# Optimization experiments

Measured on AMD Instinct MI355X. Metric: run time of the kernel, lower is better.

## Reference

```python
import jax, jax.numpy as jnp
import numpy as np

B, C, Q, H = 16, 1024, 128, 768  # batch, context_len, query_len, hidden (= proj_size)


def setup_inputs() -> dict:
    key = jax.random.key(0)
    ks = jax.random.split(key, 8)
    s = 1.0 / np.sqrt(H)
    return {
        "context": jax.random.normal(ks[0], (B, C, H), jnp.float32),
        "context_masks": jnp.ones((B, C), jnp.float32),
        "query": jax.random.normal(ks[1], (B, Q, H), jnp.float32),
        "query_masks": jnp.ones((B, Q), jnp.float32),
        "Wc": jax.random.uniform(ks[2], (H, H), jnp.float32, -s, s),   # proj_ctx weight [out,in]
        "bc": jax.random.uniform(ks[3], (H,), jnp.float32, -s, s),
        "Wq": jax.random.uniform(ks[4], (H, H), jnp.float32, -s, s),   # proj_ques weight
        "bq": jax.random.uniform(ks[5], (H,), jnp.float32, -s, s),
        "w_att": jax.random.uniform(ks[6], (H,), jnp.float32, -s, s),  # attention Linear(H,1) weight
        "b_att": jax.random.uniform(ks[7], (), jnp.float32, -s, s),
    }


def reference(context, context_masks, query, query_masks, Wc, bc, Wq, bq, w_att, b_att):
    # Projections (dropout rate = 0 -> identity)
    ctx = jnp.einsum("bch,ph->bcp", context, Wc) + bc          # [B,C,H]
    qry = jnp.einsum("bqh,ph->bqp", query, Wq) + bq            # [B,Q,H]

    # sim[b,c,q] = sum_p w_att[p]*ctx[b,c,p]*qry[b,q,p] + b_att
    # (algebraic collapse of repeat + elementwise-mul + Linear(H,1))
    sim = jnp.einsum("bcp,bqp->bcq", ctx * w_att, qry) + b_att  # [B,C,Q]

    alpha = jax.nn.softmax(sim, axis=-1)
    alpha = alpha * context_masks[:, :, None] * query_masks[:, None, :]
    a = jnp.einsum("bcq,bqp->bcp", alpha, qry)                  # [B,C,H]

    q2c = jnp.max(sim, axis=-1)                                 # [B,C]
    beta = jax.nn.softmax(q2c, axis=-1) * context_masks         # [B,C]
    b = jnp.einsum("bc,bcp->bp", beta, ctx)                     # [B,H]

    c = ctx * a
    d = ctx * b[:, None, :]
    return jnp.concatenate([ctx, a, c, d], axis=-1)             # [B,C,4H]
```

## Files before the change

### kernel.cpp

```cpp
#include <hip/hip_runtime.h>
#include <cstdint>

#define B_ 16
#define C_ 1024
#define Q_ 128
#define H_ 768
#define OSTR (4 * H_)

typedef __attribute__((ext_vector_type(8))) short bf16x8;
typedef __attribute__((ext_vector_type(4))) float f32x4;
typedef __attribute__((ext_vector_type(4))) int int4v;

__device__ __forceinline__ unsigned short f2bf(float x) {
  union { float f; unsigned u; } v; v.f = x;
  unsigned r = v.u + 0x7FFFu + ((v.u >> 16) & 1u);
  return (unsigned short)(r >> 16);
}
__device__ __forceinline__ unsigned pk2(float a, float b) {
  return (unsigned)f2bf(a) | ((unsigned)f2bf(b) << 16);
}
__device__ __forceinline__ float bf2f(unsigned short u) {
  union { unsigned u; float f; } t; t.u = ((unsigned)u) << 16; return t.f;
}

__global__ __launch_bounds__(256) void f2bf4_kernel(
    const float* __restrict__ s0, unsigned short* __restrict__ d0, int n0,
    const float* __restrict__ s1, unsigned short* __restrict__ d1, int n1,
    const float* __restrict__ s2, unsigned short* __restrict__ d2, int n2,
    const float* __restrict__ s3, unsigned short* __restrict__ d3, int n3) {
  int i = blockIdx.x * 256 + threadIdx.x;
  const float* s;
  unsigned short* d;
  if (i < n0) { s = s0; d = d0; }
  else if ((i -= n0) < n1) { s = s1; d = d1; }
  else if ((i -= n1) < n2) { s = s2; d = d2; }
  else if ((i -= n2) < n3) { s = s3; d = d3; }
  else return;
  f32x4 a = __builtin_nontemporal_load((const f32x4*)s + 2 * i);
  f32x4 b = __builtin_nontemporal_load((const f32x4*)s + 2 * i + 1);
  int4v o;
  o[0] = (int)pk2(a[0], a[1]); o[1] = (int)pk2(a[2], a[3]);
  o[2] = (int)pk2(b[0], b[1]); o[3] = (int)pk2(b[2], b[3]);
  ((int4v*)d)[i] = o;
}

template <int MODE>
__global__ __launch_bounds__(256) void gemm_uni(
    const unsigned short* __restrict__ A, const unsigned short* __restrict__ Bm,
    const float* __restrict__ bias, unsigned short* __restrict__ ob1,
    unsigned short* __restrict__ ob2, const float* __restrict__ watt,
    const float* __restrict__ cmask, const float* __restrict__ qmask,
    float* __restrict__ q2c, int K, int qchunk) {
  __shared__ __align__(16) unsigned char smem[(MODE == 0) ? 33792 : 16384];
  __shared__ float pmS[2][64];
  __shared__ float psS[2][64];
  constexpr int AROWS = (MODE < 2) ? 128 : 64;
  constexpr int MI = (MODE < 2) ? 4 : 2;
  unsigned short* As = (unsigned short*)smem;
  unsigned short* Ws = (unsigned short*)(smem + ((MODE < 2) ? 8192 : 4096));
  const int tid = threadIdx.x;
  const int lane = tid & 63;
  const int w = tid >> 6;
  const int orig = ((int)blockIdx.x & 7) * qchunk + ((int)blockIdx.x >> 3);
  const int wrA = (w >> 1) * (AROWS / 2);
  const int wcB = (w & 1) * 64;
  const int fr = lane & 15;
  const int fq = lane >> 4;

  int gm, gn, bb;
  const unsigned short *Ap, *Bp;
  if constexpr (MODE == 0 || MODE == 1) {
    gm = (orig / 6) * 128; gn = (orig % 6) * 128; bb = 0;
    Ap = A + (size_t)gm * K; Bp = Bm + (size_t)gn * K;
  } else {
    bb = orig >> 4; gm = bb * C_ + (orig & 15) * 64; gn = 0;
    Ap = A + (size_t)gm * K; Bp = Bm + (size_t)bb * Q_ * K;
  }

  auto stage128 = [&](const unsigned short* __restrict__ G, unsigned short* S, int k0) {
#pragma unroll
    for (int r = 0; r < 2; ++r) {
      const int c = r * 256 + tid;
      const int row = c >> 2, sub = c & 3;
      const unsigned short* g = G + (size_t)row * K + k0 + sub * 8;
      unsigned short* l = S + (size_t)(r * 256 + w * 64) * 8;
      __builtin_amdgcn_global_load_lds(
          (const __attribute__((address_space(1))) void*)g,
          (__attribute__((address_space(3))) void*)l, 16, 0, 0);
    }
  };
  auto stage64 = [&](const unsigned short* __restrict__ G, unsigned short* S, int k0) {
    const int c = tid;
    const int row = c >> 2, sub = c & 3;
    const unsigned short* g = G + (size_t)row * K + k0 + sub * 8;
    unsigned short* l = S + (size_t)(w * 64) * 8;
    __builtin_amdgcn_global_load_lds(
        (const __attribute__((address_space(1))) void*)g,
        (__attribute__((address_space(3))) void*)l, 16, 0, 0);
  };

  f32x4 acc[MI][4];
#pragma unroll
  for (int i = 0; i < MI; ++i)
#pragma unroll
    for (int j = 0; j < 4; ++j)
#pragma unroll
      for (int e = 0; e < 4; ++e) acc[i][j][e] = 0.f;

  for (int k0 = 0; k0 < K; k0 += 32) {
    if constexpr (MODE < 2) stage128(Ap, As, k0); else stage64(Ap, As, k0);
    stage128(Bp, Ws, k0);
    __syncthreads();
    bf16x8 af[MI], wf[4];
#pragma unroll
    for (int i = 0; i < MI; ++i)
      af[i] = *(const bf16x8*)(As + (wrA + i * 16 + fr) * 32 + fq * 8);
#pragma unroll
    for (int j = 0; j < 4; ++j)
      wf[j] = *(const bf16x8*)(Ws + (wcB + j * 16 + fr) * 32 + fq * 8);
#pragma unroll
    for (int i = 0; i < MI; ++i)
#pragma unroll
      for (int j = 0; j < 4; ++j)
        acc[i][j] = __builtin_amdgcn_mfma_f32_16x16x32_bf16(af[i], wf[j], acc[i][j], 0, 0, 0);
    __syncthreads();
  }

  if constexpr (MODE == 0) {
    unsigned short* tr16 = (unsigned short*)smem;
    float bj[4];
#pragma unroll
    for (int j = 0; j < 4; ++j) bj[j] = bias[gn + wcB + j * 16 + fr];
#pragma unroll
    for (int i = 0; i < 4; ++i)
#pragma unroll
      for (int j = 0; j < 4; ++j)
#pragma unroll
        for (int r = 0; r < 4; ++r)
          tr16[(wrA + i * 16 + fq * 4 + r) * 132 + wcB + j * 16 + fr] =
              f2bf(acc[i][j][r] + bj[j]);
    __syncthreads();
#pragma unroll
    for (int k = 0; k < 8; ++k) {
      const int f = k * 256 + tid;
      const int row = f >> 4, c8 = (f & 15) << 3;
      int4v v = *(const int4v*)&tr16[row * 132 + c8];
      *(int4v*)&ob1[(size_t)(gm + row) * H_ + gn + c8] = v;
    }
  } else if constexpr (MODE == 1) {
#pragma unroll
    for (int i = 0; i < 4; ++i) {
#pragma unroll
      for (int j = 0; j < 4; ++j) {
        const int n = gn + wcB + j * 16 + fr;
        const float bias_n = bias[n];
        const float wv = watt[n];
        ushort4 t4;
#pragma unroll
        for (int r = 0; r < 4; ++r) {
          const size_t m = (size_t)gm + wrA + i * 16 + fq * 4 + r;
          float v = acc[i][j][r] + bias_n;
          ob1[m * H_ + n] = f2bf(v * wv);
          (&t4.x)[r] = f2bf(v);
        }
        const int bidx = gm >> 7;
        const int q0 = wrA + i * 16 + fq * 4;
        *(ushort4*)(ob2 + ((size_t)bidx * H_ + n) * Q_ + q0) = t4;
      }
    }
  } else {
    float red[MI][4];
#pragma unroll
    for (int i = 0; i < MI; ++i)
#pragma unroll
      for (int r = 0; r < 4; ++r) {
        float mx = acc[i][0][r];
#pragma unroll
        for (int j = 1; j < 4; ++j) mx = fmaxf(mx, acc[i][j][r]);
        mx = fmaxf(mx, __shfl_xor(mx, 1));
        mx = fmaxf(mx, __shfl_xor(mx, 2));
        mx = fmaxf(mx, __shfl_xor(mx, 4));
        mx = fmaxf(mx, __shfl_xor(mx, 8));
        if (fr == 0) pmS[w & 1][wrA + i * 16 + fq * 4 + r] = mx;
      }
    __syncthreads();
    float qm[4];
#pragma unroll
    for (int j = 0; j < 4; ++j) qm[j] = qmask[bb * Q_ + wcB + j * 16 + fr];
#pragma unroll
    for (int i = 0; i < MI; ++i)
#pragma unroll
      for (int r = 0; r < 4; ++r) {
        const int lr = wrA + i * 16 + fq * 4 + r;
        const float M = fmaxf(pmS[0][lr], pmS[1][lr]);
        if ((w & 1) == 0 && fr == 0) q2c[gm + lr] = M;
        float s = 0.f;
#pragma unroll
        for (int j = 0; j < 4; ++j) {
          acc[i][j][r] = __expf(acc[i][j][r] - M);
          s += acc[i][j][r];
        }
        s += __shfl_xor(s, 1); s += __shfl_xor(s, 2);
        s += __shfl_xor(s, 4); s += __shfl_xor(s, 8);
        if (fr == 0) psS[w & 1][lr] = s;
      }
    __syncthreads();
#pragma unroll
    for (int i = 0; i < MI; ++i)
#pragma unroll
      for (int r = 0; r < 4; ++r) {
        const int lr = wrA + i * 16 + fq * 4 + r;
        const float S = psS[0][lr] + psS[1][lr];
        const float inv = cmask[gm + lr] / S;
#pragma unroll
        for (int j = 0; j < 4; ++j) {
          const int lc = wcB + j * 16 + fr;
          ob1[(size_t)(gm + lr) * Q_ + lc] = f2bf(acc[i][j][r] * inv * qm[j]);
        }
      }
  }
}

__global__ __launch_bounds__(256) void pv_kernel(
    const unsigned short* __restrict__ alpha, const unsigned short* __restrict__ qryT,
    const unsigned short* __restrict__ ctxp, const float* __restrict__ bvec,
    float* __restrict__ out32) {
  __shared__ __align__(16) unsigned char smem[33792];
  const int tid = threadIdx.x;
  const int lane = tid & 63;
  const int w = tid >> 6;
  const int fr = lane & 15;
  const int fq = lane >> 4;
  const int orig = ((int)blockIdx.x & 7) * 192 + ((int)blockIdx.x >> 3);
  const int bb = orig / 96;
  const int rem = orig % 96;
  const int gm = bb * C_ + (rem / 6) * 64;
  const int gn = (rem % 6) * 128;
  const unsigned short* Ap = alpha + (size_t)gm * Q_;
  const unsigned short* Bp = qryT + ((size_t)bb * H_ + gn) * Q_;
  const int wrA = (w >> 1) * 32;
  const int wcB = (w & 1) * 64;
  unsigned short* Ws = (unsigned short*)smem;

#pragma unroll
  for (int kk = 0; kk < 4; ++kk) {
#pragma unroll
    for (int r = 0; r < 2; ++r) {
      const int c = r * 256 + tid;
      const int row = c >> 2, sub = c & 3;
      const unsigned short* g = Bp + (size_t)row * Q_ + kk * 32 + sub * 8;
      unsigned short* l = Ws + kk * 4096 + (size_t)(r * 256 + w * 64) * 8;
      __builtin_amdgcn_global_load_lds(
          (const __attribute__((address_space(1))) void*)g,
          (__attribute__((address_space(3))) void*)l, 16, 0, 0);
    }
  }
  ushort4 cxr[8];
#pragma unroll
  for (int k = 0; k < 8; ++k) {
    const int f = k * 256 + tid;
    const int row = f >> 5, c4 = (f & 31) << 2;
    cxr[k] = *(const ushort4*)&ctxp[(size_t)(gm + row) * H_ + gn + c4];
  }
  bf16x8 af[2][4];
#pragma unroll
  for (int i = 0; i < 2; ++i)
#pragma unroll
    for (int kk = 0; kk < 4; ++kk)
      af[i][kk] = *(const bf16x8*)(Ap + (size_t)(wrA + i * 16 + fr) * Q_ + kk * 32 + fq * 8);

  f32x4 acc[2][4];
#pragma unroll
  for (int i = 0; i < 2; ++i)
#pragma unroll
    for (int j = 0; j < 4; ++j)
#pragma unroll
      for (int e = 0; e < 4; ++e) acc[i][j][e] = 0.f;

  __syncthreads();
#pragma unroll
  for (int kk = 0; kk < 4; ++kk) {
    bf16x8 wf[4];
#pragma unroll
    for (int j = 0; j < 4; ++j)
      wf[j] = *(const bf16x8*)(Ws + kk * 4096 + (wcB + j * 16 + fr) * 32 + fq * 8);
#pragma unroll
    for (int i = 0; i < 2; ++i)
#pragma unroll
      for (int j = 0; j < 4; ++j)
        acc[i][j] = __builtin_amdgcn_mfma_f32_16x16x32_bf16(af[i][kk], wf[j], acc[i][j], 0, 0, 0);
  }
  __syncthreads();

  float* tr = (float*)smem;
#pragma unroll
  for (int i = 0; i < 2; ++i)
#pragma unroll
    for (int j = 0; j < 4; ++j)
#pragma unroll
      for (int r = 0; r < 4; ++r)
        tr[(wrA + i * 16 + fq * 4 + r) * 132 + wcB + j * 16 + fr] = acc[i][j][r];
  __syncthreads();
#pragma unroll
  for (int k = 0; k < 8; ++k) {
    const int f = k * 256 + tid;
    const int row = f >> 5, c4 = (f & 31) << 2;
    f32x4 av = *(const f32x4*)&tr[row * 132 + c4];
    const ushort4 cu = cxr[k];
    f32x4 bv = *(const f32x4*)&bvec[bb * H_ + gn + c4];
    const float cx0 = bf2f(cu.x), cx1 = bf2f(cu.y), cx2 = bf2f(cu.z), cx3 = bf2f(cu.w);
    float* rowp = out32 + (size_t)(gm + row) * OSTR + gn;
    f32x4 cxv; cxv[0] = cx0; cxv[1] = cx1; cxv[2] = cx2; cxv[3] = cx3;
    __builtin_nontemporal_store(cxv, (f32x4*)&rowp[c4]);
    __builtin_nontemporal_store(av, (f32x4*)&rowp[H_ + c4]);
    f32x4 cc;
    cc[0] = cx0 * av[0]; cc[1] = cx1 * av[1]; cc[2] = cx2 * av[2]; cc[3] = cx3 * av[3];
    __builtin_nontemporal_store(cc, (f32x4*)&rowp[2 * H_ + c4]);
    f32x4 dd;
    dd[0] = cx0 * bv[0]; dd[1] = cx1 * bv[1]; dd[2] = cx2 * bv[2]; dd[3] = cx3 * bv[3];
    __builtin_nontemporal_store(dd, (f32x4*)&rowp[3 * H_ + c4]);
  }
}

__global__ __launch_bounds__(256) void beta_bvec_kernel(
    const unsigned short* __restrict__ ctxp, const float* __restrict__ q2c,
    const float* __restrict__ cmask, float* __restrict__ bvec) {
  __shared__ float sh[C_];
  __shared__ float red[256];
  const int tid = threadIdx.x;
  const int b = blockIdx.x / 12;
  const int p0 = (blockIdx.x % 12) * 64;
  float v[4];
  float lm = -1e30f;
#pragma unroll
  for (int i = 0; i < 4; ++i) {
    v[i] = q2c[b * C_ + i * 256 + tid];
    lm = fmaxf(lm, v[i]);
  }
  red[tid] = lm;
  __syncthreads();
  for (int off = 128; off > 0; off >>= 1) {
    if (tid < off) red[tid] = fmaxf(red[tid], red[tid + off]);
    __syncthreads();
  }
  const float m = red[0];
  __syncthreads();
  float ls = 0.f;
#pragma unroll
  for (int i = 0; i < 4; ++i) {
    float e = __expf(v[i] - m);
    sh[i * 256 + tid] = e * cmask[b * C_ + i * 256 + tid];
    ls += e;
  }
  red[tid] = ls;
  __syncthreads();
  for (int off = 128; off > 0; off >>= 1) {
    if (tid < off) red[tid] += red[tid + off];
    __syncthreads();
  }
  const float denom = red[0];
  const int pp = tid & 63;
  const int cg = tid >> 6;
  const unsigned short* base = ctxp + ((size_t)(b * C_ + cg)) * H_ + p0 + pp;
  float acc = 0.f;
#pragma unroll 4
  for (int c = cg; c < C_; c += 4) {
    acc += sh[c] * bf2f(*base);
    base += (size_t)4 * H_;
  }
  __syncthreads();
  red[tid] = acc;
  __syncthreads();
  if (tid < 64)
    bvec[b * H_ + p0 + tid] =
        (red[tid] + red[tid + 64] + red[tid + 128] + red[tid + 192]) / denom;
}

extern "C" void kernel_launch(void* const* d_in, const int* in_sizes, int n_in,
                              void* d_out, int out_size, void* d_ws, size_t ws_size,
                              hipStream_t stream) {
  const float* context = (const float*)d_in[0];
  const float* cmask   = (const float*)d_in[1];
  const float* query   = (const float*)d_in[2];
  const float* qmask   = (const float*)d_in[3];
  const float* Wc      = (const float*)d_in[4];
  const float* bc      = (const float*)d_in[5];
  const float* Wq      = (const float*)d_in[6];
  const float* bq      = (const float*)d_in[7];
  const float* w_att   = (const float*)d_in[8];
  float* out = (float*)d_out;

  unsigned short* ws_ctxb = (unsigned short*)d_ws;
  unsigned short* ws_qinb = ws_ctxb + (size_t)B_ * C_ * H_;
  unsigned short* ws_Wcb  = ws_qinb + (size_t)B_ * Q_ * H_;
  unsigned short* ws_Wqb  = ws_Wcb + (size_t)H_ * H_;
  unsigned short* ws_qryW = ws_Wqb + (size_t)H_ * H_;
  unsigned short* ws_qryT = ws_qryW + (size_t)B_ * Q_ * H_;
  unsigned short* ws_ctxp = ws_qryT + (size_t)B_ * H_ * Q_;
  float* ws_q2c  = (float*)(ws_ctxp + (size_t)B_ * C_ * H_);
  float* ws_bvec = ws_q2c + (size_t)B_ * C_;
  unsigned short* ws_alpha = ws_qinb;

  {
    const int n0 = B_ * C_ * H_ / 8;
    const int n1 = B_ * Q_ * H_ / 8;
    const int n2 = H_ * H_ / 8;
    const int n3 = n2;
    const int tot = n0 + n1 + n2 + n3;
    f2bf4_kernel<<<(tot + 255) / 256, 256, 0, stream>>>(
        context, ws_ctxb, n0, query, ws_qinb, n1, Wc, ws_Wcb, n2, Wq, ws_Wqb, n3);
  }
  gemm_uni<1><<<96, 256, 0, stream>>>(
      ws_qinb, ws_Wqb, bq, ws_qryW, ws_qryT, w_att,
      nullptr, nullptr, nullptr, H_, 12);
  gemm_uni<0><<<768, 256, 0, stream>>>(
      ws_ctxb, ws_Wcb, bc, ws_ctxp, nullptr, nullptr,
      nullptr, nullptr, nullptr, H_, 96);
  gemm_uni<2><<<256, 256, 0, stream>>>(
      ws_ctxp, ws_qryW, nullptr, ws_alpha, nullptr, nullptr,
      cmask, qmask, ws_q2c, H_, 32);
  beta_bvec_kernel<<<B_ * 12, 256, 0, stream>>>(ws_ctxp, ws_q2c, cmask, ws_bvec);
  pv_kernel<<<1536, 256, 0, stream>>>(ws_alpha, ws_qryT, ws_ctxp, ws_bvec, out);
}
```

Measured before the change: 155.1 us.

## Merge context and query projections into one launch; halve pv_kernel tile rows

The two projection GEMMs (context and query) now run as a single 864-block kernel that picks its operands by block index, so one launch replaces two and the 96 query blocks fill gaps alongside the 768 context blocks. The similarity/softmax GEMM is split out into its own specialised kernel with no logic change. pv_kernel now uses 32-row tiles instead of 64, doubling the grid to 3072 blocks and using fewer registers per block, which should help occupancy. In exchange, each Wq/qryT tile is reloaded into shared memory twice as often, and the merged kernel has a runtime branch on block role.

```diff
diff --git a/kernel.cpp b/kernel.cpp
--- a/kernel.cpp
+++ b/kernel.cpp
@@ -44,89 +44,79 @@
   ((int4v*)d)[i] = o;
 }
 
-template <int MODE>
-__global__ __launch_bounds__(256) void gemm_uni(
-    const unsigned short* __restrict__ A, const unsigned short* __restrict__ Bm,
-    const float* __restrict__ bias, unsigned short* __restrict__ ob1,
-    unsigned short* __restrict__ ob2, const float* __restrict__ watt,
-    const float* __restrict__ cmask, const float* __restrict__ qmask,
-    float* __restrict__ q2c, int K, int qchunk) {
-  __shared__ __align__(16) unsigned char smem[(MODE == 0) ? 33792 : 16384];
-  __shared__ float pmS[2][64];
-  __shared__ float psS[2][64];
-  constexpr int AROWS = (MODE < 2) ? 128 : 64;
-  constexpr int MI = (MODE < 2) ? 4 : 2;
+__global__ __launch_bounds__(256) void proj_kernel(
+    const unsigned short* __restrict__ ctxb, const unsigned short* __restrict__ Wcb,
+    const float* __restrict__ bc, unsigned short* __restrict__ ctxp,
+    const unsigned short* __restrict__ qinb, const unsigned short* __restrict__ Wqb,
+    const float* __restrict__ bq, unsigned short* __restrict__ qryW,
+    unsigned short* __restrict__ qryT, const float* __restrict__ watt) {
+  __shared__ __align__(16) unsigned char smem[33792];
   unsigned short* As = (unsigned short*)smem;
-  unsigned short* Ws = (unsigned short*)(smem + ((MODE < 2) ? 8192 : 4096));
+  unsigned short* Ws = (unsigned short*)(smem + 8192);
   const int tid = threadIdx.x;
   const int lane = tid & 63;
   const int w = tid >> 6;
-  const int orig = ((int)blockIdx.x & 7) * qchunk + ((int)blockIdx.x >> 3);
-  const int wrA = (w >> 1) * (AROWS / 2);
+  const int bid = (int)blockIdx.x;
+  const bool isC = bid < 768;
+  int orig, gm, gn;
+  const unsigned short *Ap, *Bp;
+  const float* bias;
+  if (isC) {
+    orig = (bid & 7) * 96 + (bid >> 3);
+    gm = (orig / 6) * 128; gn = (orig % 6) * 128;
+    Ap = ctxb + (size_t)gm * H_; Bp = Wcb + (size_t)gn * H_; bias = bc;
+  } else {
+    const int b2 = bid - 768;
+    orig = (b2 & 7) * 12 + (b2 >> 3);
+    gm = (orig / 6) * 128; gn = (orig % 6) * 128;
+    Ap = qinb + (size_t)gm * H_; Bp = Wqb + (size_t)gn * H_; bias = bq;
+  }
+  const int wrA = (w >> 1) * 64;
   const int wcB = (w & 1) * 64;
   const int fr = lane & 15;
   const int fq = lane >> 4;
 
-  int gm, gn, bb;
-  const unsigned short *Ap, *Bp;
-  if constexpr (MODE == 0 || MODE == 1) {
-    gm = (orig / 6) * 128; gn = (orig % 6) * 128; bb = 0;
-    Ap = A + (size_t)gm * K; Bp = Bm + (size_t)gn * K;
-  } else {
-    bb = orig >> 4; gm = bb * C_ + (orig & 15) * 64; gn = 0;
-    Ap = A + (size_t)gm * K; Bp = Bm + (size_t)bb * Q_ * K;
-  }
-
   auto stage128 = [&](const unsigned short* __restrict__ G, unsigned short* S, int k0) {
 #pragma unroll
     for (int r = 0; r < 2; ++r) {
       const int c = r * 256 + tid;
       const int row = c >> 2, sub = c & 3;
-      const unsigned short* g = G + (size_t)row * K + k0 + sub * 8;
+      const unsigned short* g = G + (size_t)row * H_ + k0 + sub * 8;
       unsigned short* l = S + (size_t)(r * 256 + w * 64) * 8;
       __builtin_amdgcn_global_load_lds(
           (const __attribute__((address_space(1))) void*)g,
           (__attribute__((address_space(3))) void*)l, 16, 0, 0);
     }
   };
-  auto stage64 = [&](const unsigned short* __restrict__ G, unsigned short* S, int k0) {
-    const int c = tid;
-    const int row = c >> 2, sub = c & 3;
-    const unsigned short* g = G + (size_t)row * K + k0 + sub * 8;
-    unsigned short* l = S + (size_t)(w * 64) * 8;
-    __builtin_amdgcn_global_load_lds(
-        (const __attribute__((address_space(1))) void*)g,
-        (__attribute__((address_space(3))) void*)l, 16, 0, 0);
-  };
-
-  f32x4 acc[MI][4];
-#pragma unroll
-  for (int i = 0; i < MI; ++i)
+
+  f32x4 acc[4][4];
+#pragma unroll
+  for (int i = 0; i < 4; ++i)
 #pragma unroll
     for (int j = 0; j < 4; ++j)
 #pragma unroll
       for (int e = 0; e < 4; ++e) acc[i][j][e] = 0.f;
 
-  for (int k0 = 0; k0 < K; k0 += 32) {
-    if constexpr (MODE < 2) stage128(Ap, As, k0); else stage64(Ap, As, k0);
+  for (int k0 = 0; k0 < H_; k0 += 32) {
+    stage128(Ap, As, k0);
     stage128(Bp, Ws, k0);
     __syncthreads();
-    bf16x8 af[MI], wf[4];
-#pragma unroll
-    for (int i = 0; i < MI; ++i)
+    bf16x8 af[4], wf[4];
+#pragma unroll
+    for (int i = 0; i < 4; ++i)
       af[i] = *(const bf16x8*)(As + (wrA + i * 16 + fr) * 32 + fq * 8);
 #pragma unroll
     for (int j = 0; j < 4; ++j)
       wf[j] = *(const bf16x8*)(Ws + (wcB + j * 16 + fr) * 32 + fq * 8);
 #pragma unroll
-    for (int i = 0; i < MI; ++i)
+    for (int i = 0; i < 4; ++i)
 #pragma unroll
       for (int j = 0; j < 4; ++j)
         acc[i][j] = __builtin_amdgcn_mfma_f32_16x16x32_bf16(af[i], wf[j], acc[i][j], 0, 0, 0);
     __syncthreads();
   }
 
-  if constexpr (MODE == 0) {
+  if (isC) {
     unsigned short* tr16 = (unsigned short*)smem;
     float bj[4];
 #pragma unroll
@@ -145,9 +135,9 @@
       const int f = k * 256 + tid;
       const int row = f >> 4, c8 = (f & 15) << 3;
       int4v v = *(const int4v*)&tr16[row * 132 + c8];
-      *(int4v*)&ob1[(size_t)(gm + row) * H_ + gn + c8] = v;
-    }
-  } else if constexpr (MODE == 1) {
+      *(int4v*)&ctxp[(size_t)(gm + row) * H_ + gn + c8] = v;
+    }
+  } else {
 #pragma unroll
     for (int i = 0; i < 4; ++i) {
 #pragma unroll
@@ -160,65 +150,131 @@
         for (int r = 0; r < 4; ++r) {
           const size_t m = (size_t)gm + wrA + i * 16 + fq * 4 + r;
           float v = acc[i][j][r] + bias_n;
-          ob1[m * H_ + n] = f2bf(v * wv);
+          qryW[m * H_ + n] = f2bf(v * wv);
           (&t4.x)[r] = f2bf(v);
         }
         const int bidx = gm >> 7;
         const int q0 = wrA + i * 16 + fq * 4;
-        *(ushort4*)(ob2 + ((size_t)bidx * H_ + n) * Q_ + q0) = t4;
+        *(ushort4*)(qryT + ((size_t)bidx * H_ + n) * Q_ + q0) = t4;
       }
     }
-  } else {
-    float red[MI][4];
-#pragma unroll
-    for (int i = 0; i < MI; ++i)
-#pragma unroll
-      for (int r = 0; r < 4; ++r) {
-        float mx = acc[i][0][r];
-#pragma unroll
-        for (int j = 1; j < 4; ++j) mx = fmaxf(mx, acc[i][j][r]);
-        mx = fmaxf(mx, __shfl_xor(mx, 1));
-        mx = fmaxf(mx, __shfl_xor(mx, 2));
-        mx = fmaxf(mx, __shfl_xor(mx, 4));
-        mx = fmaxf(mx, __shfl_xor(mx, 8));
-        if (fr == 0) pmS[w & 1][wrA + i * 16 + fq * 4 + r] = mx;
+  }
+}
+
+__global__ __launch_bounds__(256) void sim_kernel(
+    const unsigned short* __restrict__ A, const unsigned short* __restrict__ Bm,
+    unsigned short* __restrict__ alpha, const float* __restrict__ cmask,
+    const float* __restrict__ qmask, float* __restrict__ q2c) {
+  __shared__ __align__(16) unsigned char smem[16384];
+  __shared__ float pmS[2][64];
+  __shared__ float psS[2][64];
+  unsigned short* As = (unsigned short*)smem;
+  unsigned short* Ws = (unsigned short*)(smem + 4096);
+  const int tid = threadIdx.x;
+  const int lane = tid & 63;
+  const int w = tid >> 6;
+  const int orig = ((int)blockIdx.x & 7) * 32 + ((int)blockIdx.x >> 3);
+  const int bb = orig >> 4;
+  const int gm = bb * C_ + (orig & 15) * 64;
+  const int wrA = (w >> 1) * 32;
+  const int wcB = (w & 1) * 64;
+  const int fr = lane & 15;
+  const int fq = lane >> 4;
+  const unsigned short* Ap = A + (size_t)gm * H_;
+  const unsigned short* Bp = Bm + (size_t)bb * Q_ * H_;
+
+  f32x4 acc[2][4];
+#pragma unroll
+  for (int i = 0; i < 2; ++i)
+#pragma unroll
+    for (int j = 0; j < 4; ++j)
+#pragma unroll
+      for (int e = 0; e < 4; ++e) acc[i][j][e] = 0.f;
+
+  for (int k0 = 0; k0 < H_; k0 += 32) {
+    {
+      const int row = tid >> 2, sub = tid & 3;
+      const unsigned short* g = Ap + (size_t)row * H_ + k0 + sub * 8;
+      unsigned short* l = As + (size_t)(w * 64) * 8;
+      __builtin_amdgcn_global_load_lds(
+          (const __attribute__((address_space(1))) void*)g,
+          (__attribute__((address_space(3))) void*)l, 16, 0, 0);
+    }
+#pragma unroll
+    for (int r = 0; r < 2; ++r) {
+      const int c = r * 256 + tid;
+      const int row = c >> 2, sub = c & 3;
+      const unsigned short* g = Bp + (size_t)row * H_ + k0 + sub * 8;
+      unsigned short* l = Ws + (size_t)(r * 256 + w * 64) * 8;
+      __builtin_amdgcn_global_load_lds(
+          (const __attribute__((address_space(1))) void*)g,
+          (__attribute__((address_space(3))) void*)l, 16, 0, 0);
+    }
+    __syncthreads();
+    bf16x8 af[2], wf[4];
+#pragma unroll
+    for (int i = 0; i < 2; ++i)
+      af[i] = *(const bf16x8*)(As + (wrA + i * 16 + fr) * 32 + fq * 8);
+#pragma unroll
+    for (int j = 0; j < 4; ++j)
+      wf[j] = *(const bf16x8*)(Ws + (wcB + j * 16 + fr) * 32 + fq * 8);
+#pragma unroll
+    for (int i = 0; i < 2; ++i)
+#pragma unroll
+      for (int j = 0; j < 4; ++j)
+        acc[i][j] = __builtin_amdgcn_mfma_f32_16x16x32_bf16(af[i], wf[j], acc[i][j], 0, 0, 0);
+    __syncthreads();
+  }
+
+  float red[2][4];
+#pragma unroll
+  for (int i = 0; i < 2; ++i)
+#pragma unroll
+    for (int r = 0; r < 4; ++r) {
+      float mx = acc[i][0][r];
+#pragma unroll
+      for (int j = 1; j < 4; ++j) mx = fmaxf(mx, acc[i][j][r]);
+      mx = fmaxf(mx, __shfl_xor(mx, 1));
+      mx = fmaxf(mx, __shfl_xor(mx, 2));
+      mx = fmaxf(mx, __shfl_xor(mx, 4));
+      mx = fmaxf(mx, __shfl_xor(mx, 8));
+      if (fr == 0) pmS[w & 1][wrA + i * 16 + fq * 4 + r] = mx;
+    }
+  __syncthreads();
+  float qm[4];
+#pragma unroll
+  for (int j = 0; j < 4; ++j) qm[j] = qmask[bb * Q_ + wcB + j * 16 + fr];
+#pragma unroll
+  for (int i = 0; i < 2; ++i)
+#pragma unroll
+    for (int r = 0; r < 4; ++r) {
+      const int lr = wrA + i * 16 + fq * 4 + r;
+      const float M = fmaxf(pmS[0][lr], pmS[1][lr]);
+      if ((w & 1) == 0 && fr == 0) q2c[gm + lr] = M;
+      float s = 0.f;
+#pragma unroll
+      for (int j = 0; j < 4; ++j) {
+        acc[i][j][r] = __expf(acc[i][j][r] - M);
+        s += acc[i][j][r];
       }
-    __syncthreads();
-    float qm[4];
-#pragma unroll
-    for (int j = 0; j < 4; ++j) qm[j] = qmask[bb * Q_ + wcB + j * 16 + fr];
-#pragma unroll
-    for (int i = 0; i < MI; ++i)
-#pragma unroll
-      for (int r = 0; r < 4; ++r) {
-        const int lr = wrA + i * 16 + fq * 4 + r;
-        const float M = fmaxf(pmS[0][lr], pmS[1][lr]);
-        if ((w & 1) == 0 && fr == 0) q2c[gm + lr] = M;
-        float s = 0.f;
-#pragma unroll
-        for (int j = 0; j < 4; ++j) {
-          acc[i][j][r] = __expf(acc[i][j][r] - M);
-          s += acc[i][j][r];
-        }
-        s += __shfl_xor(s, 1); s += __shfl_xor(s, 2);
-        s += __shfl_xor(s, 4); s += __shfl_xor(s, 8);
-        if (fr == 0) psS[w & 1][lr] = s;
+      s += __shfl_xor(s, 1); s += __shfl_xor(s, 2);
+      s += __shfl_xor(s, 4); s += __shfl_xor(s, 8);
+      if (fr == 0) psS[w & 1][lr] = s;
+    }
+  __syncthreads();
+#pragma unroll
+  for (int i = 0; i < 2; ++i)
+#pragma unroll
+    for (int r = 0; r < 4; ++r) {
+      const int lr = wrA + i * 16 + fq * 4 + r;
+      const float S = psS[0][lr] + psS[1][lr];
+      const float inv = cmask[gm + lr] / S;
+#pragma unroll
+      for (int j = 0; j < 4; ++j) {
+        const int lc = wcB + j * 16 + fr;
+        alpha[(size_t)(gm + lr) * Q_ + lc] = f2bf(acc[i][j][r] * inv * qm[j]);
       }
-    __syncthreads();
-#pragma unroll
-    for (int i = 0; i < MI; ++i)
-#pragma unroll
-      for (int r = 0; r < 4; ++r) {
-        const int lr = wrA + i * 16 + fq * 4 + r;
-        const float S = psS[0][lr] + psS[1][lr];
-        const float inv = cmask[gm + lr] / S;
-#pragma unroll
-        for (int j = 0; j < 4; ++j) {
-          const int lc = wcB + j * 16 + fr;
-          ob1[(size_t)(gm + lr) * Q_ + lc] = f2bf(acc[i][j][r] * inv * qm[j]);
-        }
-      }
-  }
+    }
 }
 
 __global__ __launch_bounds__(256) void pv_kernel(
@@ -231,14 +287,14 @@
   const int w = tid >> 6;
   const int fr = lane & 15;
   const int fq = lane >> 4;
-  const int orig = ((int)blockIdx.x & 7) * 192 + ((int)blockIdx.x >> 3);
-  const int bb = orig / 96;
-  const int rem = orig % 96;
-  const int gm = bb * C_ + (rem / 6) * 64;
+  const int orig = ((int)blockIdx.x & 7) * 384 + ((int)blockIdx.x >> 3);
+  const int bb = orig / 192;
+  const int rem = orig % 192;
+  const int gm = bb * C_ + (rem / 6) * 32;
   const int gn = (rem % 6) * 128;
   const unsigned short* Ap = alpha + (size_t)gm * Q_;
   const unsigned short* Bp = qryT + ((size_t)bb * H_ + gn) * Q_;
-  const int wrA = (w >> 1) * 32;
+  const int wrA = (w >> 1) * 16;
   const int wcB = (w & 1) * 64;
   unsigned short* Ws = (unsigned short*)smem;
 
@@ -255,27 +311,23 @@
           (__attribute__((address_space(3))) void*)l, 16, 0, 0);
     }
   }
-  ushort4 cxr[8];
-#pragma unroll
-  for (int k = 0; k < 8; ++k) {
+  ushort4 cxr[4];
+#pragma unroll
+  for (int k = 0; k < 4; ++k) {
     const int f = k * 256 + tid;
     const int row = f >> 5, c4 = (f & 31) << 2;
     cxr[k] = *(const ushort4*)&ctxp[(size_t)(gm + row) * H_ + gn + c4];
   }
-  bf16x8 af[2][4];
-#pragma unroll
-  for (int i = 0; i < 2; ++i)
-#pragma unroll
-    for (int kk = 0; kk < 4; ++kk)
-      af[i][kk] = *(const bf16x8*)(Ap + (size_t)(wrA + i * 16 + fr) * Q_ + kk * 32 + fq * 8);
-
-  f32x4 acc[2][4];
-#pragma unroll
-  for (int i = 0; i < 2; ++i)
-#pragma unroll
-    for (int j = 0; j < 4; ++j)
-#pragma unroll
-      for (int e = 0; e < 4; ++e) acc[i][j][e] = 0.f;
+  bf16x8 af[4];
+#pragma unroll
+  for (int kk = 0; kk < 4; ++kk)
+    af[kk] = *(const bf16x8*)(Ap + (size_t)(wrA + fr) * Q_ + kk * 32 + fq * 8);
+
+  f32x4 acc[4];
+#pragma unroll
+  for (int j = 0; j < 4; ++j)
+#pragma unroll
+    for (int e = 0; e < 4; ++e) acc[j][e] = 0.f;
 
   __syncthreads();
 #pragma unroll
@@ -285,24 +337,20 @@
     for (int j = 0; j < 4; ++j)
       wf[j] = *(const bf16x8*)(Ws + kk * 4096 + (wcB + j * 16 + fr) * 32 + fq * 8);
 #pragma unroll
-    for (int i = 0; i < 2; ++i)
-#pragma unroll
-      for (int j = 0; j < 4; ++j)
-        acc[i][j] = __builtin_amdgcn_mfma_f32_16x16x32_bf16(af[i][kk], wf[j], acc[i][j], 0, 0, 0);
+    for (int j = 0; j < 4; ++j)
+      acc[j] = __builtin_amdgcn_mfma_f32_16x16x32_bf16(af[kk], wf[j], acc[j], 0, 0, 0);
   }
   __syncthreads();
 
   float* tr = (float*)smem;
 #pragma unroll
-  for (int i = 0; i < 2; ++i)
-#pragma unroll
-    for (int j = 0; j < 4; ++j)
-#pragma unroll
-      for (int r = 0; r < 4; ++r)
-        tr[(wrA + i * 16 + fq * 4 + r) * 132 + wcB + j * 16 + fr] = acc[i][j][r];
-  __syncthreads();
-#pragma unroll
-  for (int k = 0; k < 8; ++k) {
+  for (int j = 0; j < 4; ++j)
+#pragma unroll
+    for (int r = 0; r < 4; ++r)
+      tr[(wrA + fq * 4 + r) * 132 + wcB + j * 16 + fr] = acc[j][r];
+  __syncthreads();
+#pragma unroll
+  for (int k = 0; k < 4; ++k) {
     const int f = k * 256 + tid;
     const int row = f >> 5, c4 = (f & 31) << 2;
     f32x4 av = *(const f32x4*)&tr[row * 132 + c4];
@@ -410,15 +458,10 @@
     f2bf4_kernel<<<(tot + 255) / 256, 256, 0, stream>>>(
         context, ws_ctxb, n0, query, ws_qinb, n1, Wc, ws_Wcb, n2, Wq, ws_Wqb, n3);
   }
-  gemm_uni<1><<<96, 256, 0, stream>>>(
-      ws_qinb, ws_Wqb, bq, ws_qryW, ws_qryT, w_att,
-      nullptr, nullptr, nullptr, H_, 12);
-  gemm_uni<0><<<768, 256, 0, stream>>>(
-      ws_ctxb, ws_Wcb, bc, ws_ctxp, nullptr, nullptr,
-      nullptr, nullptr, nullptr, H_, 96);
-  gemm_uni<2><<<256, 256, 0, stream>>>(
-      ws_ctxp, ws_qryW, nullptr, ws_alpha, nullptr, nullptr,
-      cmask, qmask, ws_q2c, H_, 32);
+  proj_kernel<<<864, 256, 0, stream>>>(
+      ws_ctxb, ws_Wcb, bc, ws_ctxp, ws_qinb, ws_Wqb, bq, ws_qryW, ws_qryT, w_att);
+  sim_kernel<<<256, 256, 0, stream>>>(
+      ws_ctxp, ws_qryW, ws_alpha, cmask, qmask, ws_q2c);
   beta_bvec_kernel<<<B_ * 12, 256, 0, stream>>>(ws_ctxp, ws_q2c, cmask, ws_bvec);
-  pv_kernel<<<1536, 256, 0, stream>>>(ws_alpha, ws_qryT, ws_ctxp, ws_bvec, out);
-}
+  pv_kernel<<<3072, 256, 0, stream>>>(ws_alpha, ws_qryT, ws_ctxp, ws_bvec, out);
+}
```

Result: faster. 141.8 us (-8.6%).
